# Kernel tuning notes

Measured on AMD Instinct MI355X. Metric: run time of the kernel, lower is better.

The kernel has to match this reference:

```python
import jax, jax.numpy as jnp
import numpy as np

DILS = (1, 2, 4, 8)
BN_EPS = 1e-5
NORM_EPS = 1e-12


def _affinity(xn, d):
    """Cosine affinity of each pixel with its 8 dilated 3x3 neighbors.
    xn: L2-normalized features [B,C,H,W]. Zero padding => out-of-bounds affinity = 0.
    Returns [B,8,H,W] with channels in unfold (row-major window) order, center removed,
    clamped at 0 (matches `affinity[affinity < 0] = 0`).
    """
    B, C, H, W = xn.shape
    p = jnp.pad(xn, ((0, 0), (0, 0), (d, d), (d, d)))
    chans = []
    for i in range(3):
        for j in range(3):
            if i == 1 and j == 1:
                continue  # skip center (index win_h*win_w//2 == 4)
            nb = p[:, :, i * d:i * d + H, j * d:j * d + W]
            chans.append(jnp.sum(nb * xn, axis=1))
    return jnp.maximum(jnp.stack(chans, axis=1), 0.0)


def _bn_relu(x, g, b):
    # BatchNorm2d in training mode (batch statistics, biased variance), then ReLU.
    m = jnp.mean(x, axis=(0, 2, 3), keepdims=True)
    v = jnp.var(x, axis=(0, 2, 3), keepdims=True)
    y = (x - m) / jnp.sqrt(v + BN_EPS)
    return jnp.maximum(y * g[None, :, None, None] + b[None, :, None, None], 0.0)


def setup_inputs() -> dict:
    key = jax.random.key(0)
    ks = jax.random.split(key, 8)
    B, C, H, W, sfc = 4, 32, 320, 640, 32
    inp = {"x": jax.random.normal(ks[0], (B, C, H, W), dtype=jnp.float32)}
    for i in range(4):
        inp[f"w{i+1}"] = jax.random.normal(ks[1 + i], (sfc, 8), dtype=jnp.float32) * 0.1
        inp[f"g{i+1}"] = jnp.ones((sfc,), dtype=jnp.float32)
        inp[f"b{i+1}"] = jnp.zeros((sfc,), dtype=jnp.float32)
    inp["w_last"] = jax.random.normal(ks[5], (sfc, 4 * sfc, 3, 3), dtype=jnp.float32) * 0.05
    inp["g_last"] = jnp.ones((sfc,), dtype=jnp.float32)
    inp["b_last"] = jnp.zeros((sfc,), dtype=jnp.float32)
    inp["w_final"] = jax.random.normal(ks[6], (sfc, sfc), dtype=jnp.float32) * 0.1
    return inp


def reference(x, w1, g1, b1, w2, g2, b2, w3, g3, b3, w4, g4, b4,
              w_last, g_last, b_last, w_final):
    # F.normalize(x, dim=1, p=2): x / max(||x||_2, eps)
    norm = jnp.sqrt(jnp.sum(x * x, axis=1, keepdims=True))
    xn = x / jnp.maximum(norm, NORM_EPS)

    branches = ((w1, g1, b1), (w2, g2, b2), (w3, g3, b3), (w4, g4, b4))
    feats = []
    for d, (w, g, b) in zip(DILS, branches):
        a = _affinity(xn, d)                       # [B,8,H,W]
        h = jnp.einsum('bchw,oc->bohw', a, w)      # 1x1 conv, no bias
        feats.append(_bn_relu(h, g, b))            # [B,sfc,H,W]

    cat = jnp.concatenate(feats, axis=1)           # [B,4*sfc,H,W]
    h = jax.lax.conv_general_dilated(
        cat, w_last, window_strides=(1, 1), padding=((1, 1), (1, 1)),
        dimension_numbers=('NCHW', 'OIHW', 'NCHW'))
    h = _bn_relu(h, g_last, b_last)
    out = jnp.einsum('bchw,oc->bohw', h, w_final)  # final 1x1 conv, no bias
    return out
```

## Files before the change

### kernel.cpp

```cpp
#include <hip/hip_runtime.h>
#include <math.h>

#define BB 4
#define CC0 32
#define HH 320
#define WW 640
#define HWp (HH*WW)
#define CHWp (CC0*HWp)
#define NCH (BB*HWp)
#define CCAT 128

#define WT_OFF  ((size_t)0)
#define ST_OFF  ((size_t)36864)
#define SC_OFF  ((size_t)37184)
#define CATF_OFF ((size_t)37504)

typedef unsigned short ushort_t;
typedef __attribute__((ext_vector_type(8)))  short  short8;
typedef __attribute__((ext_vector_type(16))) float  float16v;

static __device__ __forceinline__ float bf2f(ushort_t u) {
  unsigned x = ((unsigned)u) << 16;
  float f; __builtin_memcpy(&f, &x, 4); return f;
}
static __device__ __forceinline__ ushort_t f2bf(float f) {
  unsigned x; __builtin_memcpy(&x, &f, 4);
  unsigned r = (x + 0x7fffu + ((x >> 16) & 1u)) >> 16;
  return (ushort_t)r;
}
static __device__ __forceinline__ unsigned pack2(float a, float b) {
  return (unsigned)f2bf(a) | ((unsigned)f2bf(b) << 16);
}
static __device__ __forceinline__ void unpack8(uint4 u, float* f) {
  f[0] = bf2f((ushort_t)(u.x & 0xffff)); f[1] = bf2f((ushort_t)(u.x >> 16));
  f[2] = bf2f((ushort_t)(u.y & 0xffff)); f[3] = bf2f((ushort_t)(u.y >> 16));
  f[4] = bf2f((ushort_t)(u.z & 0xffff)); f[5] = bf2f((ushort_t)(u.z >> 16));
  f[6] = bf2f((ushort_t)(u.w & 0xffff)); f[7] = bf2f((ushort_t)(u.w >> 16));
}

__global__ __launch_bounds__(256) void k_normalize(const float* __restrict__ x,
                                                   ushort_t* __restrict__ xnb) {
  int p2 = blockIdx.x * 256 + threadIdx.x;
  int b  = blockIdx.y;
  const float2* xp = (const float2*)(x + (size_t)b * CHWp) + p2;
  float va[32], vb[32];
  float sa = 0.f, sb = 0.f;
  #pragma unroll
  for (int c = 0; c < 32; ++c) {
    float2 v = xp[c * (HWp/2)];
    va[c] = v.x; vb[c] = v.y;
    sa = fmaf(v.x, v.x, sa); sb = fmaf(v.y, v.y, sb);
  }
  float ia = 1.f / fmaxf(sqrtf(sa), 1e-12f);
  float ib = 1.f / fmaxf(sqrtf(sb), 1e-12f);
  uint4* op = (uint4*)(xnb + ((size_t)b * HWp + (size_t)p2 * 2) * 32);
  #pragma unroll
  for (int q = 0; q < 4; ++q) {
    uint4 u;
    u.x = pack2(va[q*8+0]*ia, va[q*8+1]*ia);
    u.y = pack2(va[q*8+2]*ia, va[q*8+3]*ia);
    u.z = pack2(va[q*8+4]*ia, va[q*8+5]*ia);
    u.w = pack2(va[q*8+6]*ia, va[q*8+7]*ia);
    op[q] = u;
  }
  #pragma unroll
  for (int q = 0; q < 4; ++q) {
    uint4 u;
    u.x = pack2(vb[q*8+0]*ib, vb[q*8+1]*ib);
    u.y = pack2(vb[q*8+2]*ib, vb[q*8+3]*ib);
    u.z = pack2(vb[q*8+4]*ib, vb[q*8+5]*ib);
    u.w = pack2(vb[q*8+6]*ib, vb[q*8+7]*ib);
    op[4 + q] = u;
  }
}

__global__ __launch_bounds__(256, 4) void k_branch4(const ushort_t* __restrict__ xnb,
                                                    const float* __restrict__ w0,
                                                    const float* __restrict__ w1,
                                                    const float* __restrict__ w2,
                                                    const float* __restrict__ w3,
                                                    ushort_t* __restrict__ cat) {
  int bx = blockIdx.x;
  bx = (bx & 7) * 100 + (bx >> 3);
  int pix = bx * 256 + threadIdx.x;
  int b   = blockIdx.y;
  int y = pix / WW;
  int x = pix - y * WW;

  const ushort_t* cp0 = xnb + ((size_t)b * HWp + pix) * 32;
  float cen[32];
  {
    const uint4* cv = (const uint4*)cp0;
    uint4 c0 = cv[0], c1 = cv[1], c2 = cv[2], c3 = cv[3];
    unpack8(c0, cen); unpack8(c1, cen + 8); unpack8(c2, cen + 16); unpack8(c3, cen + 24);
  }
  uint4* cp = (uint4*)(cat + ((size_t)b * HWp + pix) * 128);

  #pragma unroll 1
  for (int z = 0; z < 4; ++z) {
    int d = 1 << z;
    const float* w = (z == 0) ? w0 : (z == 1) ? w1 : (z == 2) ? w2 : w3;
    const int DY[8] = {-1,-1,-1, 0, 0, 1, 1, 1};
    const int DX[8] = {-1, 0, 1,-1, 1,-1, 0, 1};
    float a[8];
    #pragma unroll
    for (int k = 0; k < 8; ++k) {
      int dy = DY[k] * d, dx = DX[k] * d;
      bool ok = ((unsigned)(y + dy) < (unsigned)HH) && ((unsigned)(x + dx) < (unsigned)WW);
      int ofs = ok ? (dy * WW + dx) : 0;
      const uint4* np = (const uint4*)(cp0 + (ptrdiff_t)ofs * 32);
      uint4 n0 = np[0], n1 = np[1], n2 = np[2], n3 = np[3];
      float nb[32];
      unpack8(n0, nb); unpack8(n1, nb + 8); unpack8(n2, nb + 16); unpack8(n3, nb + 24);
      float acc = 0.f;
      #pragma unroll
      for (int c = 0; c < 32; ++c) acc = fmaf(cen[c], nb[c], acc);
      a[k] = ok ? fmaxf(acc, 0.f) : 0.f;
    }
    #pragma unroll
    for (int q = 0; q < 4; ++q) {
      unsigned pw[4];
      #pragma unroll
      for (int pp = 0; pp < 4; ++pp) {
        int o = q * 8 + pp * 2;
        float h0 = 0.f, h1 = 0.f;
        #pragma unroll
        for (int k = 0; k < 8; ++k) {
          h0 = fmaf(a[k], w[o * 8 + k], h0);
          h1 = fmaf(a[k], w[(o + 1) * 8 + k], h1);
        }
        pw[pp] = pack2(h0, h1);
      }
      uint4 u; u.x = pw[0]; u.y = pw[1]; u.z = pw[2]; u.w = pw[3];
      cp[z * 4 + q] = u;
    }
  }
}

__global__ __launch_bounds__(256) void k_stats_cat(const ushort_t* __restrict__ cat,
                                                   float* __restrict__ g_s,
                                                   float* __restrict__ g_q) {
  int t  = threadIdx.x;
  int cg = t & 15;
  int pr = t >> 4;
  size_t pix0 = (size_t)blockIdx.x * 2048 + pr;
  const uint4* base = (const uint4*)cat;
  float s[8] = {0,0,0,0,0,0,0,0}, q[8] = {0,0,0,0,0,0,0,0};
  for (int j = 0; j < 128; ++j) {
    size_t pix = pix0 + (size_t)j * 16;
    uint4 u = base[pix * 16 + cg];
    float v[8]; unpack8(u, v);
    #pragma unroll
    for (int i = 0; i < 8; ++i) { s[i] += v[i]; q[i] = fmaf(v[i], v[i], q[i]); }
  }
  __shared__ float ls[16][128], lq[16][128];
  #pragma unroll
  for (int i = 0; i < 8; ++i) { ls[pr][cg*8+i] = s[i]; lq[pr][cg*8+i] = q[i]; }
  __syncthreads();
  if (t < 128) {
    float a = 0.f, bq = 0.f;
    #pragma unroll
    for (int r = 0; r < 16; ++r) { a += ls[r][t]; bq += lq[r][t]; }
    atomicAdd(g_s + t, a); atomicAdd(g_q + t, bq);
  }
}

__global__ __launch_bounds__(256) void k_stats_f32(const float* __restrict__ t,
                                                   float* __restrict__ g_s,
                                                   float* __restrict__ g_q) {
  int c = blockIdx.y, b = blockIdx.z;
  size_t base = ((size_t)b * 32 + c) * HWp + (size_t)blockIdx.x * 8192;
  const float4* p = (const float4*)(t + base) + threadIdx.x;
  float s = 0.f, q = 0.f;
  #pragma unroll
  for (int j = 0; j < 8; ++j) {
    float4 v = p[j * 256];
    s += v.x + v.y + v.z + v.w;
    q = fmaf(v.x, v.x, q); q = fmaf(v.y, v.y, q);
    q = fmaf(v.z, v.z, q); q = fmaf(v.w, v.w, q);
  }
  #pragma unroll
  for (int off = 32; off > 0; off >>= 1) {
    s += __shfl_down(s, off, 64);
    q += __shfl_down(q, off, 64);
  }
  __shared__ float ls[4], lq[4];
  int lane = threadIdx.x & 63, wid = threadIdx.x >> 6;
  if (lane == 0) { ls[wid] = s; lq[wid] = q; }
  __syncthreads();
  if (threadIdx.x == 0) {
    float ts = 0, tq = 0;
    #pragma unroll
    for (int i = 0; i < 4; ++i) { ts += ls[i]; tq += lq[i]; }
    atomicAdd(g_s + c, ts); atomicAdd(g_q + c, tq);
  }
}

__global__ void k_bnfin(const float* __restrict__ s, const float* __restrict__ q,
                        const float* g0, const float* g1, const float* g2, const float* g3,
                        const float* b0, const float* b1, const float* b2, const float* b3,
                        float* __restrict__ scale, float* __restrict__ shift, int Cc) {
  int c = threadIdx.x;
  if (c >= Cc) return;
  const float* g; const float* bb; int ci;
  if (Cc == 128) {
    int z = c >> 5; ci = c & 31;
    g  = (z == 0) ? g0 : (z == 1) ? g1 : (z == 2) ? g2 : g3;
    bb = (z == 0) ? b0 : (z == 1) ? b1 : (z == 2) ? b2 : b3;
  } else { g = g0; bb = b0; ci = c; }
  float mean = s[c] / (float)NCH;
  float var  = q[c] / (float)NCH - mean * mean;
  float inv  = 1.f / sqrtf(var + 1e-5f);
  float scv  = g[ci] * inv;
  scale[c] = scv;
  shift[c] = bb[ci] - mean * scv;
}

__global__ void k_wt(const float* __restrict__ wl, ushort_t* __restrict__ wbf) {
  int idx = blockIdx.x * 256 + threadIdx.x;
  if (idx >= 9 * 8 * 64 * 8) return;
  int j = idx & 7;
  int l = (idx >> 3) & 63;
  int tc = idx >> 9;
  int t = tc >> 3, cg = tc & 7;
  int o = l & 31;
  int ch = cg * 16 + ((l >> 5) << 3) + j;
  wbf[idx] = f2bf(wl[(o * 128 + ch) * 9 + t]);
}

#define SROWS 6
#define SCOLS 34
#define CHPAD 72
__global__ __launch_bounds__(256, 4) void k_conv(const ushort_t* __restrict__ cat,
                                                 const ushort_t* __restrict__ wbf,
                                                 const float* __restrict__ scale,
                                                 const float* __restrict__ shift,
                                                 float* __restrict__ out) {
  __shared__ __align__(16) ushort_t s_in[SROWS * SCOLS * CHPAD];
  int lane = threadIdx.x;
  int w    = threadIdx.y;
  int tid  = w * 64 + lane;
  int gx0 = blockIdx.x * 32, gy0 = blockIdx.y * 4;
  int b = blockIdx.z;
  size_t bHW = (size_t)b * HWp;

  const short8* wfr = (const short8*)wbf;
  float16v acc = {};

  int site0 = tid >> 3;
  int chp   = tid & 7;

  #pragma unroll
  for (int r = 0; r < 2; ++r) {
    int chb = r * 64 + chp * 8;
    float4 sc0 = *(const float4*)&scale[chb];
    float4 sc1 = *(const float4*)&scale[chb + 4];
    float4 sh0 = *(const float4*)&shift[chb];
    float4 sh1 = *(const float4*)&shift[chb + 4];
    float scl[8] = {sc0.x,sc0.y,sc0.z,sc0.w,sc1.x,sc1.y,sc1.z,sc1.w};
    float shf[8] = {sh0.x,sh0.y,sh0.z,sh0.w,sh1.x,sh1.y,sh1.z,sh1.w};

    if (r) __syncthreads();
    for (int s = site0; s < SROWS * SCOLS; s += 32) {
      int row = s / SCOLS, col = s - row * SCOLS;
      int gy = gy0 - 1 + row, gx = gx0 - 1 + col;
      uint4 u = {0u,0u,0u,0u};
      if ((unsigned)gy < (unsigned)HH && (unsigned)gx < (unsigned)WW) {
        uint4 raw = *(const uint4*)&cat[(bHW + (size_t)gy * WW + gx) * 128 + chb];
        unsigned rw[4] = {raw.x, raw.y, raw.z, raw.w};
        unsigned pk[4];
        #pragma unroll
        for (int q = 0; q < 4; ++q) {
          float v0 = fmaxf(fmaf(bf2f((ushort_t)(rw[q] & 0xffff)), scl[q*2],   shf[q*2]),   0.f);
          float v1 = fmaxf(fmaf(bf2f((ushort_t)(rw[q] >> 16)),    scl[q*2+1], shf[q*2+1]), 0.f);
          pk[q] = pack2(v0, v1);
        }
        u.x = pk[0]; u.y = pk[1]; u.z = pk[2]; u.w = pk[3];
      }
      *(uint4*)&s_in[(size_t)s * CHPAD + chp * 8] = u;
    }
    __syncthreads();

    int pcol = lane & 31;
    int half = lane >> 5;
    #pragma unroll
    for (int t = 0; t < 9; ++t) {
      int ky = t / 3, kx = t - ky * 3;
      int rowbase = ((w + ky) * SCOLS + pcol + kx) * CHPAD + half * 8;
      #pragma unroll
      for (int c = 0; c < 4; ++c) {
        short8 bfrag = wfr[(t * 8 + r * 4 + c) * 64 + lane];
        short8 afrag = *(const short8*)&s_in[rowbase + c * 16];
        acc = __builtin_amdgcn_mfma_f32_32x32x16_bf16(afrag, bfrag, acc, 0, 0, 0);
      }
    }
  }

  __syncthreads();
  float* epi = (float*)s_in + w * (32 * 33);
  int half = lane >> 5, mm = lane & 31;
  #pragma unroll
  for (int r16 = 0; r16 < 16; ++r16) {
    int m = (r16 & 3) + 8 * (r16 >> 2) + 4 * half;
    epi[m * 33 + mm] = acc[r16];
  }
  __syncthreads();
  size_t obase = bHW + (size_t)(gy0 + w) * WW + gx0 + mm;
  #pragma unroll
  for (int i = 0; i < 16; ++i) {
    int o = half * 16 + i;
    out[(size_t)o * HWp + obase + (size_t)b * (CHWp - HWp)] = epi[mm * 33 + o];
  }
}

__global__ __launch_bounds__(256) void k_final(const float* hin,
                                               const float* __restrict__ wf,
                                               const float* __restrict__ scale,
                                               const float* __restrict__ shift,
                                               float* out) {
  int p2 = blockIdx.x * 256 + threadIdx.x;
  int b  = blockIdx.y;
  const float2* hp = (const float2*)(hin + (size_t)b * CHWp) + p2;
  float va[32], vb[32];
  #pragma unroll
  for (int c = 0; c < 32; ++c) {
    float2 v = hp[c * (HWp/2)];
    va[c] = fmaxf(fmaf(v.x, scale[c], shift[c]), 0.f);
    vb[c] = fmaxf(fmaf(v.y, scale[c], shift[c]), 0.f);
  }
  float2* op = (float2*)(out + (size_t)b * CHWp) + p2;
  #pragma unroll
  for (int o = 0; o < 32; ++o) {
    float ra = 0.f, rb = 0.f;
    #pragma unroll
    for (int c = 0; c < 32; ++c) {
      float wv = wf[o * 32 + c];
      ra = fmaf(va[c], wv, ra);
      rb = fmaf(vb[c], wv, rb);
    }
    float2 rr; rr.x = ra; rr.y = rb;
    op[o * (HWp/2)] = rr;
  }
}

extern "C" void kernel_launch(void* const* d_in, const int* in_sizes, int n_in,
                              void* d_out, int out_size, void* d_ws, size_t ws_size,
                              hipStream_t stream) {
  const float* x      = (const float*)d_in[0];
  const float* w1     = (const float*)d_in[1];
  const float* g1     = (const float*)d_in[2];
  const float* b1     = (const float*)d_in[3];
  const float* w2     = (const float*)d_in[4];
  const float* g2     = (const float*)d_in[5];
  const float* b2     = (const float*)d_in[6];
  const float* w3     = (const float*)d_in[7];
  const float* g3     = (const float*)d_in[8];
  const float* b3     = (const float*)d_in[9];
  const float* w4     = (const float*)d_in[10];
  const float* g4     = (const float*)d_in[11];
  const float* b4     = (const float*)d_in[12];
  const float* w_last = (const float*)d_in[13];
  const float* g_last = (const float*)d_in[14];
  const float* b_last = (const float*)d_in[15];
  const float* w_fin  = (const float*)d_in[16];

  float* ws = (float*)d_ws;
  ushort_t* wbf = (ushort_t*)(ws + WT_OFF);
  float*    st  = ws + ST_OFF;
  float*    sc  = ws + SC_OFF;
  ushort_t* cat = (ushort_t*)(ws + CATF_OFF);

  ushort_t* xnb = (ushort_t*)d_out;
  float*    xn  = (float*)d_out;

  hipMemsetAsync(st, 0, 320 * sizeof(float), stream);

  k_normalize<<<dim3(400, 4), 256, 0, stream>>>(x, xnb);
  k_branch4<<<dim3(800, 4), 256, 0, stream>>>(xnb, w1, w2, w3, w4, cat);
  k_stats_cat<<<400, 256, 0, stream>>>(cat, st, st + 128);
  k_bnfin<<<1, 128, 0, stream>>>(st, st + 128, g1, g2, g3, g4, b1, b2, b3, b4,
                                 sc, sc + 128, 128);
  k_wt<<<144, 256, 0, stream>>>(w_last, wbf);
  k_conv<<<dim3(20, 80, 4), dim3(64, 4), 0, stream>>>(cat, wbf, sc, sc + 128, xn);
  k_stats_f32<<<dim3(25, 32, 4), 256, 0, stream>>>(xn, st + 256, st + 288);
  k_bnfin<<<1, 128, 0, stream>>>(st + 256, st + 288, g_last, g_last, g_last, g_last,
                                 b_last, b_last, b_last, b_last, sc + 256, sc + 288, 32);
  k_final<<<dim3(400, 4), 256, 0, stream>>>(xn, w_fin, sc + 256, sc + 288, (float*)d_out);
}
```

Before: 698.8 us.

## Store normalized features as fp32 and split branch kernel per dilation

The normalize kernel now writes fp32 channels-last features instead of bf16, which doubles that intermediate's footprint but removes the unpack step. The branch kernel is split across a third grid dimension, one dilation per block. This gives four times as many blocks and fewer live values per thread, at the cost of reloading the center pixel per dilation. Cat output is written with nontemporal stores, and the per-neighbor dot product uses four partial accumulators. Affinities are now computed from fp32 rather than bf16 inputs.

Result: slower. 1.185 ms (+69.6%).

```diff
diff --git a/kernel.cpp b/kernel.cpp
--- a/kernel.cpp
+++ b/kernel.cpp
@@ -18,6 +18,7 @@
 typedef unsigned short ushort_t;
 typedef __attribute__((ext_vector_type(8)))  short  short8;
 typedef __attribute__((ext_vector_type(16))) float  float16v;
+typedef __attribute__((ext_vector_type(4)))  unsigned uintv4;
 
 static __device__ __forceinline__ float bf2f(ushort_t u) {
   unsigned x = ((unsigned)u) << 16;
@@ -39,7 +40,7 @@
 }
 
 __global__ __launch_bounds__(256) void k_normalize(const float* __restrict__ x,
-                                                   ushort_t* __restrict__ xnb) {
+                                                   float* __restrict__ xnf) {
   int p2 = blockIdx.x * 256 + threadIdx.x;
   int b  = blockIdx.y;
   const float2* xp = (const float2*)(x + (size_t)b * CHWp) + p2;
@@ -53,33 +54,32 @@
   }
   float ia = 1.f / fmaxf(sqrtf(sa), 1e-12f);
   float ib = 1.f / fmaxf(sqrtf(sb), 1e-12f);
-  uint4* op = (uint4*)(xnb + ((size_t)b * HWp + (size_t)p2 * 2) * 32);
-  #pragma unroll
-  for (int q = 0; q < 4; ++q) {
-    uint4 u;
-    u.x = pack2(va[q*8+0]*ia, va[q*8+1]*ia);
-    u.y = pack2(va[q*8+2]*ia, va[q*8+3]*ia);
-    u.z = pack2(va[q*8+4]*ia, va[q*8+5]*ia);
-    u.w = pack2(va[q*8+6]*ia, va[q*8+7]*ia);
+  float4* op = (float4*)(xnf + ((size_t)b * HWp + (size_t)p2 * 2) * 32);
+  #pragma unroll
+  for (int q = 0; q < 8; ++q) {
+    float4 u;
+    u.x = va[q*4+0]*ia; u.y = va[q*4+1]*ia;
+    u.z = va[q*4+2]*ia; u.w = va[q*4+3]*ia;
     op[q] = u;
   }
   #pragma unroll
-  for (int q = 0; q < 4; ++q) {
-    uint4 u;
-    u.x = pack2(vb[q*8+0]*ib, vb[q*8+1]*ib);
-    u.y = pack2(vb[q*8+2]*ib, vb[q*8+3]*ib);
-    u.z = pack2(vb[q*8+4]*ib, vb[q*8+5]*ib);
-    u.w = pack2(vb[q*8+6]*ib, vb[q*8+7]*ib);
-    op[4 + q] = u;
-  }
-}
-
-__global__ __launch_bounds__(256, 4) void k_branch4(const ushort_t* __restrict__ xnb,
-                                                    const float* __restrict__ w0,
-                                                    const float* __restrict__ w1,
-                                                    const float* __restrict__ w2,
-                                                    const float* __restrict__ w3,
-                                                    ushort_t* __restrict__ cat) {
+  for (int q = 0; q < 8; ++q) {
+    float4 u;
+    u.x = vb[q*4+0]*ib; u.y = vb[q*4+1]*ib;
+    u.z = vb[q*4+2]*ib; u.w = vb[q*4+3]*ib;
+    op[8 + q] = u;
+  }
+}
+
+__global__ __launch_bounds__(256, 4) void k_branch(const float* __restrict__ xnf,
+                                                   const float* __restrict__ w0,
+                                                   const float* __restrict__ w1,
+                                                   const float* __restrict__ w2,
+                                                   const float* __restrict__ w3,
+                                                   ushort_t* __restrict__ cat) {
+  int z = blockIdx.z;
+  int d = 1 << z;
+  const float* w = (z == 0) ? w0 : (z == 1) ? w1 : (z == 2) ? w2 : w3;
   int bx = blockIdx.x;
   bx = (bx & 7) * 100 + (bx >> 3);
   int pix = bx * 256 + threadIdx.x;
@@ -87,53 +87,54 @@
   int y = pix / WW;
   int x = pix - y * WW;
 
-  const ushort_t* cp0 = xnb + ((size_t)b * HWp + pix) * 32;
-  float cen[32];
+  const float* cp0 = xnf + ((size_t)b * HWp + pix) * 32;
+  float4 cen[8];
   {
-    const uint4* cv = (const uint4*)cp0;
-    uint4 c0 = cv[0], c1 = cv[1], c2 = cv[2], c3 = cv[3];
-    unpack8(c0, cen); unpack8(c1, cen + 8); unpack8(c2, cen + 16); unpack8(c3, cen + 24);
-  }
-  uint4* cp = (uint4*)(cat + ((size_t)b * HWp + pix) * 128);
-
-  #pragma unroll 1
-  for (int z = 0; z < 4; ++z) {
-    int d = 1 << z;
-    const float* w = (z == 0) ? w0 : (z == 1) ? w1 : (z == 2) ? w2 : w3;
-    const int DY[8] = {-1,-1,-1, 0, 0, 1, 1, 1};
-    const int DX[8] = {-1, 0, 1,-1, 1,-1, 0, 1};
-    float a[8];
-    #pragma unroll
-    for (int k = 0; k < 8; ++k) {
-      int dy = DY[k] * d, dx = DX[k] * d;
-      bool ok = ((unsigned)(y + dy) < (unsigned)HH) && ((unsigned)(x + dx) < (unsigned)WW);
-      int ofs = ok ? (dy * WW + dx) : 0;
-      const uint4* np = (const uint4*)(cp0 + (ptrdiff_t)ofs * 32);
-      uint4 n0 = np[0], n1 = np[1], n2 = np[2], n3 = np[3];
-      float nb[32];
-      unpack8(n0, nb); unpack8(n1, nb + 8); unpack8(n2, nb + 16); unpack8(n3, nb + 24);
-      float acc = 0.f;
+    const float4* cv = (const float4*)cp0;
+    #pragma unroll
+    for (int q = 0; q < 8; ++q) cen[q] = cv[q];
+  }
+
+  const int DY[8] = {-1,-1,-1, 0, 0, 1, 1, 1};
+  const int DX[8] = {-1, 0, 1,-1, 1,-1, 0, 1};
+  float a[8];
+  #pragma unroll
+  for (int k = 0; k < 8; ++k) {
+    int dy = DY[k] * d, dx = DX[k] * d;
+    bool ok = ((unsigned)(y + dy) < (unsigned)HH) && ((unsigned)(x + dx) < (unsigned)WW);
+    int ofs = ok ? (dy * WW + dx) : 0;
+    const float4* np = (const float4*)(cp0 + (ptrdiff_t)ofs * 32);
+    float a0 = 0.f, a1 = 0.f, a2 = 0.f, a3 = 0.f;
+    #pragma unroll
+    for (int q = 0; q < 8; ++q) {
+      float4 n = np[q];
+      a0 = fmaf(cen[q].x, n.x, a0);
+      a1 = fmaf(cen[q].y, n.y, a1);
+      a2 = fmaf(cen[q].z, n.z, a2);
+      a3 = fmaf(cen[q].w, n.w, a3);
+    }
+    float acc = (a0 + a1) + (a2 + a3);
+    a[k] = ok ? fmaxf(acc, 0.f) : 0.f;
+  }
+
+  uintv4* cp = (uintv4*)(cat + ((size_t)b * HWp + pix) * 128 + z * 32);
+  #pragma unroll
+  for (int q = 0; q < 4; ++q) {
+    unsigned pw[4];
+    #pragma unroll
+    for (int pp = 0; pp < 4; ++pp) {
+      int o = q * 8 + pp * 2;
+      float h0 = 0.f, h1 = 0.f;
       #pragma unroll
-      for (int c = 0; c < 32; ++c) acc = fmaf(cen[c], nb[c], acc);
-      a[k] = ok ? fmaxf(acc, 0.f) : 0.f;
-    }
-    #pragma unroll
-    for (int q = 0; q < 4; ++q) {
-      unsigned pw[4];
-      #pragma unroll
-      for (int pp = 0; pp < 4; ++pp) {
-        int o = q * 8 + pp * 2;
-        float h0 = 0.f, h1 = 0.f;
-        #pragma unroll
-        for (int k = 0; k < 8; ++k) {
-          h0 = fmaf(a[k], w[o * 8 + k], h0);
-          h1 = fmaf(a[k], w[(o + 1) * 8 + k], h1);
-        }
-        pw[pp] = pack2(h0, h1);
+      for (int k = 0; k < 8; ++k) {
+        h0 = fmaf(a[k], w[o * 8 + k], h0);
+        h1 = fmaf(a[k], w[(o + 1) * 8 + k], h1);
       }
-      uint4 u; u.x = pw[0]; u.y = pw[1]; u.z = pw[2]; u.w = pw[3];
-      cp[z * 4 + q] = u;
-    }
+      pw[pp] = pack2(h0, h1);
+    }
+    uintv4 u;
+    u.x = pw[0]; u.y = pw[1]; u.z = pw[2]; u.w = pw[3];
+    __builtin_nontemporal_store(u, cp + q);
   }
 }
 
@@ -370,13 +371,12 @@
   float*    sc  = ws + SC_OFF;
   ushort_t* cat = (ushort_t*)(ws + CATF_OFF);
 
-  ushort_t* xnb = (ushort_t*)d_out;
-  float*    xn  = (float*)d_out;
+  float* xn = (float*)d_out;
 
   hipMemsetAsync(st, 0, 320 * sizeof(float), stream);
 
-  k_normalize<<<dim3(400, 4), 256, 0, stream>>>(x, xnb);
-  k_branch4<<<dim3(800, 4), 256, 0, stream>>>(xnb, w1, w2, w3, w4, cat);
+  k_normalize<<<dim3(400, 4), 256, 0, stream>>>(x, xn);
+  k_branch<<<dim3(800, 4, 4), 256, 0, stream>>>(xn, w1, w2, w3, w4, cat);
   k_stats_cat<<<400, 256, 0, stream>>>(cat, st, st + 128);
   k_bnfin<<<1, 128, 0, stream>>>(st, st + 128, g1, g2, g3, g4, b1, b2, b3, b4,
                                  sc, sc + 128, 128);
```
